# Performance work log

Hardware: AMD Instinct MI355X
Metric: run time of the kernel (lower is better)

## Reference

```python
import jax, jax.numpy as jnp
import numpy as np

B, N, D, H = 8, 1024, 768, 12
HD = D // H  # head_dim = 64


def setup_inputs() -> dict:
    key = jax.random.key(0)
    k1, k2 = jax.random.split(key)
    x = jax.random.normal(k1, (B, N, D), dtype=jnp.float32)
    W_qkv = jax.random.normal(k2, (D, 3 * D), dtype=jnp.float32) * 0.02
    b_qkv = jnp.zeros((3 * D,), dtype=jnp.float32)
    return {"x": x, "W_qkv": W_qkv, "b_qkv": b_qkv}


def reference(x, W_qkv, b_qkv):
    b, n, d = x.shape
    qkv = x @ W_qkv + b_qkv                      # [B, N, 3D]
    qkv = qkv.reshape(b, n, 3, H, HD)
    qkv = jnp.transpose(qkv, (2, 0, 3, 1, 4))    # [3, B, H, N, HD]
    q, k, v = qkv[0], qkv[1], qkv[2]
    scale = 1.0 / jnp.sqrt(jnp.float32(HD))
    scores = jnp.einsum('bhqd,bhkd->bhqk', q, k) * scale   # [B, H, N, N]
    attn = jax.nn.softmax(scores, axis=-1)
    out = jnp.einsum('bhqk,bhkd->bhqd', attn, v)            # [B, H, N, HD]
    # concat heads along last dim (same as torch.cat over head outputs)
    return jnp.transpose(out, (0, 2, 1, 3)).reshape(b, n, d)
```

## Files before the change

### kernel.cpp

```cpp
#include <hip/hip_runtime.h>
#include <stdint.h>

#define BB 8
#define NN 1024
#define DDIM 768
#define HH 12
#define HDIM 64
#define D3 2304
#define MM 8192

typedef __attribute__((ext_vector_type(4))) float f32x4;
typedef __attribute__((ext_vector_type(16))) float f32x16;
typedef __attribute__((ext_vector_type(8))) __bf16 bf16x8;
typedef __attribute__((ext_vector_type(8))) unsigned short u16x8;
typedef __attribute__((ext_vector_type(4))) unsigned short u16x4;

__device__ __forceinline__ unsigned short f2bf(float f) {
  unsigned int u = __float_as_uint(f);
  u += 0x7FFFu + ((u >> 16) & 1u);
  return (unsigned short)(u >> 16);
}

__device__ __forceinline__ void gload_lds16(const void* g, void* l) {
  __builtin_amdgcn_global_load_lds((const __attribute__((address_space(1))) void*)g,
                                   (__attribute__((address_space(3))) void*)l,
                                   16, 0, 0);
}

__device__ __forceinline__ unsigned cvtpk_bf16(float lo, float hi) {
  unsigned r;
  asm("v_cvt_pk_bf16_f32 %0, %1, %2" : "=v"(r) : "v"(lo), "v"(hi));
  return r;
}

__device__ __forceinline__ bf16x8 mkfrag(unsigned a, unsigned b, unsigned c, unsigned d) {
  union { unsigned u[4]; bf16x8 v; } x;
  x.u[0] = a; x.u[1] = b; x.u[2] = c; x.u[3] = d;
  return x.v;
}

#if __has_builtin(__builtin_amdgcn_exp2f)
#define EXP2(x) __builtin_amdgcn_exp2f(x)
#else
#define EXP2(x) exp2f(x)
#endif

#define QSCL 0.18033688f

__global__ void k_prep(const float4* __restrict__ x, u16x4* __restrict__ xb,
                       const float* __restrict__ W, unsigned short* __restrict__ Wt) {
  __shared__ float tile[32][33];
  const int bid = blockIdx.x;
  if (bid < 6144) {
    int i = bid * 256 + threadIdx.x;
    float4 v = x[i];
    u16x4 o;
    o[0] = f2bf(v.x); o[1] = f2bf(v.y); o[2] = f2bf(v.z); o[3] = f2bf(v.w);
    xb[i] = o;
    return;
  }
  const int bid2 = bid - 6144;
  const int tx = threadIdx.x & 31, ty = threadIdx.x >> 5;
  const int n0 = (bid2 % 72) * 32;
  const int k0 = (bid2 / 72) * 32;
  for (int i = 0; i < 4; ++i) {
    int k = k0 + ty + i * 8;
    tile[ty + i * 8][tx] = W[(size_t)k * D3 + n0 + tx];
  }
  __syncthreads();
  for (int i = 0; i < 4; ++i) {
    int n = n0 + ty + i * 8;
    Wt[(size_t)n * DDIM + k0 + tx] = f2bf(tile[tx][ty + i * 8]);
  }
}

__global__ __launch_bounds__(256, 2)
void k_gemm(const unsigned short* __restrict__ A, const unsigned short* __restrict__ Bt,
            const float* __restrict__ bias, unsigned short* __restrict__ C) {
  __shared__ char lds[64 * 1024];
  const int t = threadIdx.x, lane = t & 63, wid = t >> 6;
  const int orig = blockIdx.x;
  const int wg = (orig & 7) * 144 + (orig >> 3);
  const int m0 = (wg & 63) * 128, n0 = (wg >> 6) * 128;
  const int wr = wid >> 1, wc = wid & 1;
  const int grp = lane >> 4, lc = lane & 15;

  f32x4 acc[4][4];
  for (int i = 0; i < 4; ++i)
    for (int j = 0; j < 4; ++j) acc[i][j] = (f32x4)(0.0f);

  auto STAGE = [&](int buf, int kt) {
    char* Ab = lds + buf * 32768;
    char* Bb = Ab + 16384;
#pragma unroll
    for (int i = 0; i < 4; ++i) {
      int id = wid * 4 + i;
      int row = id * 8 + (lane >> 3);
      int cs = ((lane & 7) << 4) ^ ((row & 7) << 4);
      gload_lds16((const char*)A + (size_t)(m0 + row) * 1536 + kt * 128 + cs, Ab + id * 1024);
      gload_lds16((const char*)Bt + (size_t)(n0 + row) * 1536 + kt * 128 + cs, Bb + id * 1024);
    }
  };

  STAGE(0, 0);
  for (int kt = 0; kt < 12; ++kt) {
    if (kt < 11) {
      STAGE((kt + 1) & 1, kt + 1);
      asm volatile("s_waitcnt vmcnt(8)" ::: "memory");
    } else {
      asm volatile("s_waitcnt vmcnt(0)" ::: "memory");
    }
    __builtin_amdgcn_s_barrier();

    const char* As = lds + (kt & 1) * 32768;
    const char* Bs = As + 16384;
    bf16x8 af[4][2], bfr[4][2];
#pragma unroll
    for (int f = 0; f < 4; ++f)
#pragma unroll
      for (int kk = 0; kk < 2; ++kk) {
        int ra = wr * 64 + f * 16 + lc;
        af[f][kk] = *(const bf16x8*)(As + ra * 128 + ((kk * 64 + grp * 16) ^ ((ra & 7) << 4)));
        int rb = wc * 64 + f * 16 + lc;
        bfr[f][kk] = *(const bf16x8*)(Bs + rb * 128 + ((kk * 64 + grp * 16) ^ ((rb & 7) << 4)));
      }
    __builtin_amdgcn_s_setprio(1);
#pragma unroll
    for (int mf = 0; mf < 4; ++mf)
#pragma unroll
      for (int nf = 0; nf < 4; ++nf) {
        acc[mf][nf] = __builtin_amdgcn_mfma_f32_16x16x32_bf16(af[mf][0], bfr[nf][0], acc[mf][nf], 0, 0, 0);
        acc[mf][nf] = __builtin_amdgcn_mfma_f32_16x16x32_bf16(af[mf][1], bfr[nf][1], acc[mf][nf], 0, 0, 0);
      }
    __builtin_amdgcn_s_setprio(0);
    __builtin_amdgcn_s_barrier();
  }

  float bv[4];
  float qs[4];
  for (int nf = 0; nf < 4; ++nf) {
    bv[nf] = bias[n0 + wc * 64 + nf * 16 + lc];
    qs[nf] = (n0 + wc * 64 + nf * 16) < DDIM ? QSCL : 1.0f;
  }
  for (int mf = 0; mf < 4; ++mf)
    for (int nf = 0; nf < 4; ++nf)
      for (int i = 0; i < 4; ++i) {
        int r = m0 + wr * 64 + mf * 16 + grp * 4 + i;
        int c = n0 + wc * 64 + nf * 16 + lc;
        C[(size_t)r * D3 + c] = f2bf((acc[mf][nf][i] + bv[nf]) * qs[nf]);
      }
}

__global__ void k_pack(const unsigned short* __restrict__ qkv,
                       unsigned short* __restrict__ kp, unsigned short* __restrict__ vp) {
  __shared__ unsigned short KT[64][68];
  __shared__ unsigned short VT[64][68];
  const int bh = blockIdx.x, kt = blockIdx.y;
  const int b = bh / HH, h = bh % HH;
  const int n0 = kt * 64;
  const int t = threadIdx.x;
#pragma unroll
  for (int it = 0; it < 2; ++it) {
    int id = it * 256 + t;
    int row = id >> 3, seg = id & 7;
    const unsigned short* src = qkv + (size_t)(b * NN + n0 + row) * D3 + DDIM + h * HDIM + seg * 8;
    *(u16x8*)&KT[row][seg * 8] = *(const u16x8*)src;
    *(u16x8*)&VT[row][seg * 8] = *(const u16x8*)(src + DDIM);
  }
  __syncthreads();
  const size_t base = (size_t)(bh * 16 + kt) * 4096;
#pragma unroll
  for (int it = 0; it < 2; ++it) {
    int w = it * 256 + t;
    int c = w >> 6, lane = w & 63;
    int hi2 = lane >> 5, l31 = lane & 31;
    int half = c & 1, quad = c >> 1;
    {
      int row = half * 32 + l31, seg = quad * 2 + hi2;
      *(u16x8*)(kp + base + (size_t)w * 8) = *(const u16x8*)&KT[row][seg * 8];
    }
    {
      int d = half * 32 + l31, nloc = quad * 16 + hi2 * 8;
      u16x8 o;
#pragma unroll
      for (int j = 0; j < 8; ++j) o[j] = VT[nloc + j][d];
      *(u16x8*)(vp + base + (size_t)w * 8) = o;
    }
  }
}

__global__ __launch_bounds__(256, 3)
void k_attn(const unsigned short* __restrict__ qkv,
            const unsigned short* __restrict__ kp, const unsigned short* __restrict__ vp,
            float* __restrict__ out) {
  __shared__ char lds[48 * 1024];
  const int lane = threadIdx.x & 63, wid = threadIdx.x >> 6;
  const int orig = blockIdx.x;
  const int wg = (orig & 7) * 96 + (orig >> 3);
  const int bh = wg >> 3, qt = wg & 7;
  const int b = bh / HH, h = bh % HH;
  const int q0 = qt * 128 + wid * 32;
  const int l31 = lane & 31, hi = lane >> 5;

  auto STAGE = [&](int bi, int kt2) {
    char* buf = lds + bi * 16384;
    const char* gk = (const char*)kp + (size_t)(bh * 16 + kt2) * 8192 + lane * 16;
    const char* gv = (const char*)vp + (size_t)(bh * 16 + kt2) * 8192 + lane * 16;
#pragma unroll
    for (int i = 0; i < 4; ++i) {
      int e = wid * 4 + i;
      const char* g = (e < 8) ? (gk + e * 1024) : (gv + (e - 8) * 1024);
      char* l = (e < 8) ? (buf + e * 1024) : (buf + 8192 + (e - 8) * 1024);
      gload_lds16(g, l);
    }
  };

  STAGE(0, 0);

  bf16x8 qf[4];
  const char* qbase = (const char*)qkv + ((size_t)(b * NN + q0 + l31) * D3 + h * HDIM) * 2;
#pragma unroll
  for (int ds_ = 0; ds_ < 4; ++ds_)
    qf[ds_] = *(const bf16x8*)(qbase + ds_ * 32 + hi * 16);

  f32x16 acc0 = (f32x16)(0.0f), acc1 = (f32x16)(0.0f);
  float l = 0.0f;

  asm volatile("s_waitcnt vmcnt(0)" ::: "memory");
  __builtin_amdgcn_s_barrier();

  int cur = 0;
  for (int kt = 0; kt < 16; ++kt) {
    const int nxt = (cur == 2) ? 0 : cur + 1;
    if (kt < 15) {
      STAGE(nxt, kt + 1);
      asm volatile("s_waitcnt vmcnt(4)" ::: "memory");
    } else {
      asm volatile("s_waitcnt vmcnt(0)" ::: "memory");
    }
    __builtin_amdgcn_s_barrier();

    const char* Kc = lds + cur * 16384;
    const char* Vc = Kc + 8192;

    bf16x8 kf[4][2];
#pragma unroll
    for (int ds_ = 0; ds_ < 4; ++ds_)
#pragma unroll
      for (int r = 0; r < 2; ++r)
        kf[ds_][r] = *(const bf16x8*)(Kc + (ds_ * 2 + r) * 1024 + lane * 16);

    f32x16 st0 = (f32x16)(0.0f), st1 = (f32x16)(0.0f);
    __builtin_amdgcn_s_setprio(1);
#pragma unroll
    for (int ds_ = 0; ds_ < 4; ++ds_) {
      st0 = __builtin_amdgcn_mfma_f32_32x32x16_bf16(kf[ds_][0], qf[ds_], st0, 0, 0, 0);
      st1 = __builtin_amdgcn_mfma_f32_32x32x16_bf16(kf[ds_][1], qf[ds_], st1, 0, 0, 0);
    }
    __builtin_amdgcn_s_setprio(0);

    bf16x8 vf[4][2];
#pragma unroll
    for (int cc = 0; cc < 4; ++cc)
#pragma unroll
      for (int r = 0; r < 2; ++r)
        vf[cc][r] = *(const bf16x8*)(Vc + (cc * 2 + r) * 1024 + lane * 16);

    float s0 = 0.f, s1 = 0.f, s2 = 0.f, s3 = 0.f;
#pragma unroll
    for (int i = 0; i < 16; i += 4) {
      float p0 = EXP2(st0[i]);
      float p1 = EXP2(st0[i + 1]);
      float p2 = EXP2(st0[i + 2]);
      float p3 = EXP2(st0[i + 3]);
      st0[i] = p0; st0[i + 1] = p1; st0[i + 2] = p2; st0[i + 3] = p3;
      s0 += p0; s1 += p1; s2 += p2; s3 += p3;
    }
#pragma unroll
    for (int i = 0; i < 16; i += 4) {
      float p0 = EXP2(st1[i]);
      float p1 = EXP2(st1[i + 1]);
      float p2 = EXP2(st1[i + 2]);
      float p3 = EXP2(st1[i + 3]);
      st1[i] = p0; st1[i + 1] = p1; st1[i + 2] = p2; st1[i + 3] = p3;
      s0 += p0; s1 += p1; s2 += p2; s3 += p3;
    }
    l += (s0 + s1) + (s2 + s3);

#pragma unroll
    for (int kblk = 0; kblk < 2; ++kblk) {
      const f32x16& sp = kblk ? st1 : st0;
      unsigned c0 = cvtpk_bf16(sp[0], sp[1]),   c1 = cvtpk_bf16(sp[2], sp[3]);
      unsigned c2 = cvtpk_bf16(sp[4], sp[5]),   c3 = cvtpk_bf16(sp[6], sp[7]);
      unsigned c4 = cvtpk_bf16(sp[8], sp[9]),   c5 = cvtpk_bf16(sp[10], sp[11]);
      unsigned c6 = cvtpk_bf16(sp[12], sp[13]), c7 = cvtpk_bf16(sp[14], sp[15]);
      unsigned z0 = hi ? c0 : c2, z1 = hi ? c1 : c3;
      unsigned z2 = hi ? c4 : c6, z3 = hi ? c5 : c7;
      unsigned w0 = __shfl_xor(z0, 32, 64), w1 = __shfl_xor(z1, 32, 64);
      unsigned w2 = __shfl_xor(z2, 32, 64), w3 = __shfl_xor(z3, 32, 64);
      bf16x8 pf0 = mkfrag(hi ? w0 : c0, hi ? w1 : c1, hi ? c2 : w0, hi ? c3 : w1);
      bf16x8 pf1 = mkfrag(hi ? w2 : c4, hi ? w3 : c5, hi ? c6 : w2, hi ? c7 : w3);

      __builtin_amdgcn_s_setprio(1);
#pragma unroll
      for (int ch = 0; ch < 2; ++ch) {
        const int cc = kblk * 2 + ch;
        const bf16x8 pf = ch ? pf1 : pf0;
        acc0 = __builtin_amdgcn_mfma_f32_32x32x16_bf16(vf[cc][0], pf, acc0, 0, 0, 0);
        acc1 = __builtin_amdgcn_mfma_f32_32x32x16_bf16(vf[cc][1], pf, acc1, 0, 0, 0);
      }
      __builtin_amdgcn_s_setprio(0);
    }

    cur = nxt;
  }

  float lf = l + __shfl_xor(l, 32, 64);
  float inv = 1.0f / lf;
  float* obase = out + (size_t)(b * NN + q0 + l31) * DDIM + h * HDIM + hi * 4;
#pragma unroll
  for (int rq = 0; rq < 4; ++rq) {
    f32x4 o;
    o[0] = acc0[rq * 4] * inv; o[1] = acc0[rq * 4 + 1] * inv;
    o[2] = acc0[rq * 4 + 2] * inv; o[3] = acc0[rq * 4 + 3] * inv;
    *(f32x4*)(obase + rq * 8) = o;
  }
#pragma unroll
  for (int rq = 0; rq < 4; ++rq) {
    f32x4 o;
    o[0] = acc1[rq * 4] * inv; o[1] = acc1[rq * 4 + 1] * inv;
    o[2] = acc1[rq * 4 + 2] * inv; o[3] = acc1[rq * 4 + 3] * inv;
    *(f32x4*)(obase + 32 + rq * 8) = o;
  }
}

extern "C" void kernel_launch(void* const* d_in, const int* in_sizes, int n_in,
                              void* d_out, int out_size, void* d_ws, size_t ws_size,
                              hipStream_t stream) {
  const float* x = (const float*)d_in[0];
  const float* W = (const float*)d_in[1];
  const float* bqkv = (const float*)d_in[2];
  float* out = (float*)d_out;
  char* ws = (char*)d_ws;

  const size_t XB_OFF = 0;
  const size_t WT_OFF = 12582912;
  const size_t QKV_OFF = WT_OFF + 3538944;
  const size_t VP_OFF = QKV_OFF + 37748736;
  unsigned short* xb = (unsigned short*)(ws + XB_OFF);
  unsigned short* wt = (unsigned short*)(ws + WT_OFF);
  unsigned short* qkvb = (unsigned short*)(ws + QKV_OFF);
  unsigned short* kpk = (unsigned short*)(ws + XB_OFF);
  unsigned short* vpk = (unsigned short*)(ws + VP_OFF);

  k_prep<<<dim3(6144 + 1728), dim3(256), 0, stream>>>((const float4*)x, (u16x4*)xb, W, wt);
  k_gemm<<<dim3(1152), dim3(256), 0, stream>>>(xb, wt, bqkv, qkvb);
  k_pack<<<dim3(BB * HH, NN / 64), dim3(256), 0, stream>>>(qkvb, kpk, vpk);
  k_attn<<<dim3(768), dim3(256), 0, stream>>>(qkvb, kpk, vpk, out);
}
```

Baseline: 100.9 us.

## Use triple-buffered BK=32 GEMM pipeline with one barrier per step and XCD-aware tiling

The QKV GEMM now walks K in 32-element steps across three LDS buffers instead of 64-element steps across two. This cuts LDS to 48KB so three blocks can share a CU, and drops the trailing barrier each iteration. The tile mapping is also changed so each XCD owns a contiguous strip of M tiles, which should improve L2 reuse of A. The cost is twice as many K iterations with less MFMA work per barrier, and LDS reads are no longer swizzled, so bank conflicts may appear.

```diff
diff --git a/kernel.cpp b/kernel.cpp
--- a/kernel.cpp
+++ b/kernel.cpp
@@ -74,14 +74,15 @@
   }
 }
 
-__global__ __launch_bounds__(256, 2)
+__global__ __launch_bounds__(256, 3)
 void k_gemm(const unsigned short* __restrict__ A, const unsigned short* __restrict__ Bt,
             const float* __restrict__ bias, unsigned short* __restrict__ C) {
-  __shared__ char lds[64 * 1024];
+  __shared__ char lds[48 * 1024];
   const int t = threadIdx.x, lane = t & 63, wid = t >> 6;
   const int orig = blockIdx.x;
-  const int wg = (orig & 7) * 144 + (orig >> 3);
-  const int m0 = (wg & 63) * 128, n0 = (wg >> 6) * 128;
+  const int xcd = orig & 7, tt = orig >> 3;
+  const int m0 = (xcd * 8 + (tt & 7)) * 128;
+  const int n0 = (tt >> 3) * 128;
   const int wr = wid >> 1, wc = wid & 1;
   const int grp = lane >> 4, lc = lane & 15;
 
@@ -90,50 +91,49 @@
     for (int j = 0; j < 4; ++j) acc[i][j] = (f32x4)(0.0f);
 
   auto STAGE = [&](int buf, int kt) {
-    char* Ab = lds + buf * 32768;
-    char* Bb = Ab + 16384;
-#pragma unroll
-    for (int i = 0; i < 4; ++i) {
-      int id = wid * 4 + i;
-      int row = id * 8 + (lane >> 3);
-      int cs = ((lane & 7) << 4) ^ ((row & 7) << 4);
-      gload_lds16((const char*)A + (size_t)(m0 + row) * 1536 + kt * 128 + cs, Ab + id * 1024);
-      gload_lds16((const char*)Bt + (size_t)(n0 + row) * 1536 + kt * 128 + cs, Bb + id * 1024);
+    char* Ab = lds + buf * 16384;
+    char* Bb = Ab + 8192;
+#pragma unroll
+    for (int i = 0; i < 2; ++i) {
+      int chunk = wid * 2 + i;
+      int g = chunk * 64 + lane;
+      int row = g >> 2, c16 = (g & 3) << 4;
+      gload_lds16((const char*)A + (size_t)(m0 + row) * 1536 + kt * 64 + c16, Ab + chunk * 1024);
+      gload_lds16((const char*)Bt + (size_t)(n0 + row) * 1536 + kt * 64 + c16, Bb + chunk * 1024);
     }
   };
 
   STAGE(0, 0);
-  for (int kt = 0; kt < 12; ++kt) {
-    if (kt < 11) {
-      STAGE((kt + 1) & 1, kt + 1);
-      asm volatile("s_waitcnt vmcnt(8)" ::: "memory");
+  asm volatile("s_waitcnt vmcnt(0)" ::: "memory");
+  __builtin_amdgcn_s_barrier();
+
+  int cur = 0;
+  for (int kt = 0; kt < 24; ++kt) {
+    const int nxt = (cur == 2) ? 0 : cur + 1;
+    if (kt < 23) {
+      STAGE(nxt, kt + 1);
+      asm volatile("s_waitcnt vmcnt(4)" ::: "memory");
     } else {
       asm volatile("s_waitcnt vmcnt(0)" ::: "memory");
     }
     __builtin_amdgcn_s_barrier();
 
-    const char* As = lds + (kt & 1) * 32768;
-    const char* Bs = As + 16384;
-    bf16x8 af[4][2], bfr[4][2];
-#pragma unroll
-    for (int f = 0; f < 4; ++f)
-#pragma unroll
-      for (int kk = 0; kk < 2; ++kk) {
-        int ra = wr * 64 + f * 16 + lc;
-        af[f][kk] = *(const bf16x8*)(As + ra * 128 + ((kk * 64 + grp * 16) ^ ((ra & 7) << 4)));
-        int rb = wc * 64 + f * 16 + lc;
-        bfr[f][kk] = *(const bf16x8*)(Bs + rb * 128 + ((kk * 64 + grp * 16) ^ ((rb & 7) << 4)));
-      }
+    const char* As = lds + cur * 16384;
+    const char* Bs = As + 8192;
+    bf16x8 af[4], bfr[4];
+#pragma unroll
+    for (int f = 0; f < 4; ++f) {
+      af[f]  = *(const bf16x8*)(As + (wr * 64 + f * 16 + lc) * 64 + grp * 16);
+      bfr[f] = *(const bf16x8*)(Bs + (wc * 64 + f * 16 + lc) * 64 + grp * 16);
+    }
     __builtin_amdgcn_s_setprio(1);
 #pragma unroll
     for (int mf = 0; mf < 4; ++mf)
 #pragma unroll
-      for (int nf = 0; nf < 4; ++nf) {
-        acc[mf][nf] = __builtin_amdgcn_mfma_f32_16x16x32_bf16(af[mf][0], bfr[nf][0], acc[mf][nf], 0, 0, 0);
-        acc[mf][nf] = __builtin_amdgcn_mfma_f32_16x16x32_bf16(af[mf][1], bfr[nf][1], acc[mf][nf], 0, 0, 0);
-      }
+      for (int nf = 0; nf < 4; ++nf)
+        acc[mf][nf] = __builtin_amdgcn_mfma_f32_16x16x32_bf16(af[mf], bfr[nf], acc[mf][nf], 0, 0, 0);
     __builtin_amdgcn_s_setprio(0);
-    __builtin_amdgcn_s_barrier();
+    cur = nxt;
   }
 
   float bv[4];
```

Result: faster. 97.63 us (-3.2%).
